# Kernel optimization log

Hardware: AMD Instinct MI355X
Metric: run time of the kernel (lower is better)

Reference implementation:

```python
import jax, jax.numpy as jnp
import numpy as np

N_NODES = 200000
N_EDGES = 3200000
N_GRAPHS = 64
IN_DIM, HIDDEN, OUT_DIM = 128, 16, 64


def setup_inputs() -> dict:
    key = jax.random.key(0)
    ks = jax.random.split(key, 5)
    x = jax.random.normal(ks[0], (N_NODES, IN_DIM), dtype=jnp.float32)
    edge_index = jax.random.randint(ks[1], (2, N_EDGES), 0, N_NODES, dtype=jnp.int64)
    batch = jnp.sort(jax.random.randint(ks[2], (N_NODES,), 0, N_GRAPHS, dtype=jnp.int64))
    W1 = jax.random.normal(ks[3], (IN_DIM, HIDDEN), dtype=jnp.float32) * (1.0 / np.sqrt(IN_DIM))
    W2 = jax.random.normal(ks[4], (HIDDEN, OUT_DIM), dtype=jnp.float32) * (1.0 / np.sqrt(HIDDEN))
    b1 = jnp.zeros((HIDDEN,), jnp.float32)
    b2 = jnp.zeros((OUT_DIM,), jnp.float32)
    return {"x": x, "edge_index": edge_index, "batch": batch,
            "W1": W1, "b1": b1, "W2": W2, "b2": b2, "training": 0}


def _gcn_conv(x, W, b, row, col, n_nodes):
    # PyG GCNConv: add-self-loop symmetric normalization, transform then
    # gather-from-row / scatter-add-to-col.  (row, col) already include self-loops.
    h = x @ W                                             # [N, out]
    deg = jnp.zeros((n_nodes,), h.dtype).at[col].add(1.0)  # degree incl. self-loop (>=1)
    dinv = deg ** -0.5
    norm = dinv[row] * dinv[col]                          # [E+N]
    out = jnp.zeros((n_nodes, W.shape[1]), h.dtype).at[col].add(h[row] * norm[:, None])
    return out + b


def reference(x, edge_index, batch, W1, b1, W2, b2, training):
    n = x.shape[0]
    loops = jnp.arange(n, dtype=edge_index.dtype)
    row = jnp.concatenate([edge_index[0], loops])
    col = jnp.concatenate([edge_index[1], loops])
    h = _gcn_conv(x, W1, b1, row, col, n)
    h = jax.nn.relu(h)
    # F.dropout with training=False is identity (reference is deterministic)
    h = _gcn_conv(h, W2, b2, row, col, n)
    # per-graph sum pooling: replaces the Python torch.where loop
    graph_embeds = jax.ops.segment_sum(h, batch, num_segments=N_GRAPHS)
    return graph_embeds
```

## Files before the change

kernel.cpp:

```cpp
#include <hip/hip_runtime.h>


#define TPB 256
#define CHUNK 4096
#define BK_SHIFT 9
#define NPB 512
#define W1S 20

__device__ __forceinline__ float bf2f(unsigned short u) {
    union { unsigned int i; float f; } v; v.i = ((unsigned int)u) << 16; return v.f;
}
__device__ __forceinline__ unsigned short f2bf(float f) {
    union { float f; unsigned int i; } v; v.f = f;
    unsigned int r = v.i + 0x7fff + ((v.i >> 16) & 1);
    return (unsigned short)(r >> 16);
}
__device__ __forceinline__ void bfacc8(uint4 v, unsigned int m, float* a) {
    union { unsigned int i; float f; } lo, hi;
    v.x &= m; v.y &= m; v.z &= m; v.w &= m;
    lo.i = v.x << 16; hi.i = v.x & 0xffff0000u; a[0] += lo.f; a[1] += hi.f;
    lo.i = v.y << 16; hi.i = v.y & 0xffff0000u; a[2] += lo.f; a[3] += hi.f;
    lo.i = v.z << 16; hi.i = v.z & 0xffff0000u; a[4] += lo.f; a[5] += hi.f;
    lo.i = v.w << 16; hi.i = v.w & 0xffff0000u; a[6] += lo.f; a[7] += hi.f;
}
__device__ __forceinline__ void bfunp8(uint4 v, float* a) {
    union { unsigned int i; float f; } lo, hi;
    lo.i = v.x << 16; hi.i = v.x & 0xffff0000u; a[0] = lo.f; a[1] = hi.f;
    lo.i = v.y << 16; hi.i = v.y & 0xffff0000u; a[2] = lo.f; a[3] = hi.f;
    lo.i = v.z << 16; hi.i = v.z & 0xffff0000u; a[4] = lo.f; a[5] = hi.f;
    lo.i = v.w << 16; hi.i = v.w & 0xffff0000u; a[6] = lo.f; a[7] = hi.f;
}

__global__ __launch_bounds__(TPB) void hist_kernel(const int* __restrict__ col,
                                                   int* __restrict__ counts,
                                                   int E, int nblk, int nbuck) {
    __shared__ int hist[512];
    int t = threadIdx.x;
    for (int i = t; i < nbuck; i += TPB) hist[i] = 0;
    __syncthreads();
    int e0 = blockIdx.x * CHUNK;
    for (int i = t; i < CHUNK; i += TPB) {
        int e = e0 + i;
        if (e < E) atomicAdd(&hist[col[e] >> BK_SHIFT], 1);
    }
    __syncthreads();
    for (int i = t; i < nbuck; i += TPB) counts[i * nblk + blockIdx.x] = hist[i];
}

__global__ __launch_bounds__(TPB) void scan1_kernel(const int* __restrict__ in,
                                                    int* __restrict__ out,
                                                    int* __restrict__ bsum, int L) {
    __shared__ int s[TPB];
    int t = threadIdx.x;
    int i = blockIdx.x * TPB + t;
    int d = (i < L) ? in[i] : 0;
    s[t] = d; __syncthreads();
    for (int off = 1; off < TPB; off <<= 1) {
        int v = (t >= off) ? s[t - off] : 0;
        __syncthreads();
        s[t] += v;
        __syncthreads();
    }
    if (i < L) out[i] = s[t] - d;
    if (t == TPB - 1) bsum[blockIdx.x] = s[t];
}

__global__ __launch_bounds__(1024) void scan2_kernel(int* __restrict__ bsum, int nb) {
    __shared__ int s[1024];
    int t = threadIdx.x;
    int i0 = t * 2, i1 = t * 2 + 1;
    int v0 = (i0 < nb) ? bsum[i0] : 0;
    int v1 = (i1 < nb) ? bsum[i1] : 0;
    int pv = v0 + v1;
    s[t] = pv; __syncthreads();
    for (int off = 1; off < 1024; off <<= 1) {
        int u = (t >= off) ? s[t - off] : 0;
        __syncthreads();
        s[t] += u;
        __syncthreads();
    }
    int exc = s[t] - pv;
    if (i0 < nb) bsum[i0] = exc;
    if (i1 < nb) bsum[i1] = exc + v0;
}

__device__ __forceinline__ int cbase_at(const int* counts, const int* bsum, int f) {
    return counts[f] + bsum[f >> 8];
}

__global__ __launch_bounds__(TPB) void s1c_gemm_kernel(
        const int* __restrict__ row, const int* __restrict__ col,
        const int* __restrict__ counts, const int* __restrict__ bsum,
        int E, int nblk, int nbuck,
        int* __restrict__ bucketed,
        const float* __restrict__ x, const float* __restrict__ W1,
        unsigned short* __restrict__ h1b, int N, int nbg) {
    __shared__ __align__(16) char sbuf[2048 + 2048 + 8192 + 64];
    int* slhist = (int*)sbuf;
    int* sgd    = (int*)(sbuf + 2048);
    unsigned short* ssidx = (unsigned short*)(sbuf + 4096);
    int* swtot  = (int*)(sbuf + 4096 + 8192);
    float* w1s  = (float*)sbuf;

    int b = (int)blockIdx.x, t = threadIdx.x;
    int M = min(nblk, nbg);
    int role, id;
    if (b < 2 * M) { role = b & 1; id = b >> 1; }
    else           { role = (nblk > nbg) ? 0 : 1; id = b - M; }

    if (role == 0) {
        int e0 = id * CHUNK;
        int nE = min(CHUNK, E - e0);
        int Ltot = nbuck * nblk;
        int lane = t & 63, w = t >> 6;
        int bk0 = 2 * t, bk1 = 2 * t + 1;
        int cb0 = 0, cb1 = 0, c0 = 0, c1 = 0;
        if (bk0 < nbuck) {
            int f = bk0 * nblk + id;
            cb0 = cbase_at(counts, bsum, f);
            int nx = (f + 1 < Ltot) ? cbase_at(counts, bsum, f + 1) : E;
            c0 = nx - cb0;
        }
        if (bk1 < nbuck) {
            int f = bk1 * nblk + id;
            cb1 = cbase_at(counts, bsum, f);
            int nx = (f + 1 < Ltot) ? cbase_at(counts, bsum, f + 1) : E;
            c1 = nx - cb1;
        }
        int s = c0 + c1;
        int v = s;
#pragma unroll
        for (int d = 1; d < 64; d <<= 1) {
            int u2 = __shfl_up(v, d, 64);
            if (lane >= d) v += u2;
        }
        if (lane == 63) swtot[w] = v;
        __syncthreads();
        int wbase = 0;
#pragma unroll
        for (int i = 0; i < 4; ++i) wbase += (i < w) ? swtot[i] : 0;
        int o0 = wbase + v - s;
        int o1 = o0 + c0;
        if (bk0 < nbuck) { slhist[bk0] = o0; sgd[bk0] = cb0 - o0; }
        if (bk1 < nbuck) { slhist[bk1] = o1; sgd[bk1] = cb1 - o1; }
        __syncthreads();
        for (int i = t; i < nE; i += TPB) {
            int c = col[e0 + i];
            int lp = atomicAdd(&slhist[c >> BK_SHIFT], 1);
            ssidx[lp] = (unsigned short)i;
        }
        __syncthreads();
        for (int j = t; j < nE; j += TPB) {
            int i = ssidx[j];
            int c = col[e0 + i];
            int r = row[e0 + i];
            bucketed[sgd[c >> BK_SHIFT] + j] = ((c & (NPB - 1)) << 18) | r;
        }
        return;
    }
    for (int i = t; i < 128 * 16; i += TPB)
        w1s[(i >> 4) * W1S + (i & 15)] = W1[i];
    __syncthreads();
    int g = t >> 2, q = t & 3;
    int n = id * 64 + g;
    int nc = min(n, N - 1);
    const float4* xr = (const float4*)(x + (size_t)nc * 128);
    float4 xv[8];
#pragma unroll
    for (int i = 0; i < 8; ++i) xv[i] = xr[i * 4 + q];
    float acc[16];
#pragma unroll
    for (int k = 0; k < 16; ++k) acc[k] = 0.f;
#pragma unroll
    for (int i = 0; i < 8; ++i) {
        float xj[4] = {xv[i].x, xv[i].y, xv[i].z, xv[i].w};
#pragma unroll
        for (int j = 0; j < 4; ++j) {
            int k = i * 16 + q * 4 + j;
            const float4* w4 = (const float4*)&w1s[k * W1S];
            float4 wa = w4[0], wb = w4[1], wc = w4[2], wd = w4[3];
            float xc = xj[j];
            acc[0]  = fmaf(xc, wa.x, acc[0]);  acc[1]  = fmaf(xc, wa.y, acc[1]);
            acc[2]  = fmaf(xc, wa.z, acc[2]);  acc[3]  = fmaf(xc, wa.w, acc[3]);
            acc[4]  = fmaf(xc, wb.x, acc[4]);  acc[5]  = fmaf(xc, wb.y, acc[5]);
            acc[6]  = fmaf(xc, wb.z, acc[6]);  acc[7]  = fmaf(xc, wb.w, acc[7]);
            acc[8]  = fmaf(xc, wc.x, acc[8]);  acc[9]  = fmaf(xc, wc.y, acc[9]);
            acc[10] = fmaf(xc, wc.z, acc[10]); acc[11] = fmaf(xc, wc.w, acc[11]);
            acc[12] = fmaf(xc, wd.x, acc[12]); acc[13] = fmaf(xc, wd.y, acc[13]);
            acc[14] = fmaf(xc, wd.z, acc[14]); acc[15] = fmaf(xc, wd.w, acc[15]);
        }
    }
#pragma unroll
    for (int d = 1; d < 4; d <<= 1) {
#pragma unroll
        for (int k = 0; k < 16; ++k) acc[k] += __shfl_xor(acc[k], d, 4);
    }
    if (n < N) {
        unsigned int u0 = (unsigned int)f2bf(acc[4 * q]) |
                          ((unsigned int)f2bf(acc[4 * q + 1]) << 16);
        unsigned int u1 = (unsigned int)f2bf(acc[4 * q + 2]) |
                          ((unsigned int)f2bf(acc[4 * q + 3]) << 16);
        *(uint2*)&h1b[(size_t)n * 16 + 4 * q] = make_uint2(u0, u1);
    }
}

__global__ __launch_bounds__(TPB) void sort_kernel(
        const int* __restrict__ bucketed,
        const int* __restrict__ counts, const int* __restrict__ bsum,
        int E, int nblk, int nbuck,
        int* __restrict__ csr, int* __restrict__ offs, float* __restrict__ dinv,
        const unsigned short* __restrict__ h1b, unsigned short* __restrict__ h1p, int N) {
    __shared__ int lhist[NPB];
    __shared__ int part[TPB];
    __shared__ float sdinv[NPB];
    int bk = blockIdx.x, t = threadIdx.x;
    int n0 = bk << BK_SHIFT;
    int n1 = min(n0 + NPB, N);
    int e0 = cbase_at(counts, bsum, bk * nblk);
    int e1 = (bk + 1 < nbuck) ? cbase_at(counts, bsum, (bk + 1) * nblk) : E;

    lhist[t] = 0; lhist[t + TPB] = 0;
    __syncthreads();
    for (int i = e0 + t; i < e1; i += TPB)
        atomicAdd(&lhist[bucketed[i] >> 18], 1);
    __syncthreads();

    int base = t * 2;
    int c0 = lhist[base], c1 = lhist[base + 1];
    int s = c0 + c1;
    part[t] = s;
    __syncthreads();
    for (int off = 1; off < TPB; off <<= 1) {
        int v = (t >= off) ? part[t - off] : 0;
        __syncthreads();
        part[t] += v;
        __syncthreads();
    }
    int o0 = e0 + part[t] - s;
    int o1 = o0 + c0;
    lhist[base] = o0; lhist[base + 1] = o1;
    sdinv[base]     = rsqrtf((float)c0 + 1.0f);
    sdinv[base + 1] = rsqrtf((float)c1 + 1.0f);
    int n = n0 + base;
    if (n + 0 < N) { offs[n + 0] = o0; dinv[n + 0] = sdinv[base]; }
    if (n + 1 < N) { offs[n + 1] = o1; dinv[n + 1] = sdinv[base + 1]; }
    __syncthreads();

    for (int i = e0 + t; i < e1; i += TPB) {
        int v = bucketed[i];
        int pos = atomicAdd(&lhist[v >> 18], 1);
        csr[pos] = v & 0x3FFFF;
    }
    int nq = (n1 - n0) * 4;
    for (int i = t; i < nq; i += TPB) {
        float dv = sdinv[i >> 2];
        uint2 u = ((const uint2*)h1b)[(size_t)n0 * 4 + i];
        float f0 = bf2f((unsigned short)(u.x & 0xffff));
        float f1 = bf2f((unsigned short)(u.x >> 16));
        float f2 = bf2f((unsigned short)(u.y & 0xffff));
        float f3 = bf2f((unsigned short)(u.y >> 16));
        ((ushort4*)h1p)[(size_t)n0 * 4 + i] =
            make_ushort4(f2bf(f0 * dv), f2bf(f1 * dv), f2bf(f2 * dv), f2bf(f3 * dv));
    }
    if (bk == 0 && t == 0) offs[N] = E;
}

__global__ __launch_bounds__(TPB) void gather1_kernel(const int* __restrict__ csr,
                                                      const int* __restrict__ offs,
                                                      const unsigned short* __restrict__ h1p,
                                                      const float* __restrict__ dinv,
                                                      const float* __restrict__ b1,
                                                      unsigned short* __restrict__ h2p, int N) {
    int t = threadIdx.x;
    int c = blockIdx.x * 16 + (t >> 4);
    int l = t & 15;
    int half = l & 1;
    int sub  = l >> 1;
    if (c >= N) return;
    int p0 = offs[c], p1 = offs[c + 1];
    float a[8];
#pragma unroll
    for (int k = 0; k < 8; ++k) a[k] = 0.f;
    for (int p = p0; p < p1; p += 16) {
        int s16 = csr[min(p + l, p1 - 1)];
#pragma unroll
        for (int h = 0; h < 2; ++h) {
            int e = 8 * h + sub;
            int src = __shfl(s16, e, 16);
            unsigned int m = ((p + e) < p1) ? 0xffffffffu : 0u;
            uint4 v = *(const uint4*)&h1p[(size_t)src * 16 + 8 * half];
            bfacc8(v, m, a);
        }
    }
#pragma unroll
    for (int d = 2; d < 16; d <<= 1) {
#pragma unroll
        for (int k = 0; k < 8; ++k) a[k] += __shfl_xor(a[k], d, 16);
    }
    if (l < 2) {
        float dc = dinv[c];
        uint4 sv = *(const uint4*)&h1p[(size_t)c * 16 + 8 * l];
        float sf[8];
        bfunp8(sv, sf);
        unsigned int uo[4];
#pragma unroll
        for (int q = 0; q < 4; ++q) {
            float r0 = fmaf(dc, a[2 * q] + sf[2 * q], b1[8 * l + 2 * q]);
            float r1 = fmaf(dc, a[2 * q + 1] + sf[2 * q + 1], b1[8 * l + 2 * q + 1]);
            r0 = dc * fmaxf(r0, 0.f);
            r1 = dc * fmaxf(r1, 0.f);
            uo[q] = (unsigned int)f2bf(r0) | ((unsigned int)f2bf(r1) << 16);
        }
        *(uint4*)&h2p[(size_t)c * 16 + 8 * l] = make_uint4(uo[0], uo[1], uo[2], uo[3]);
    }
}

__global__ __launch_bounds__(TPB) void gather2f_kernel(
        const int* __restrict__ csr, const int* __restrict__ offs,
        const unsigned short* __restrict__ h2p, const float* __restrict__ dinv,
        const float* __restrict__ W2, const float* __restrict__ b2,
        const int* __restrict__ batch, float* __restrict__ out, int N) {
    __shared__ float w2s[16 * 64];
    __shared__ float asT[64 * 17];
    __shared__ float pool[64];
    int t = threadIdx.x;
    for (int i = t; i < 16 * 64; i += TPB) w2s[i] = W2[i];
    if (t < 64) pool[t] = 0.f;

    int n0 = blockIdx.x * 64;
    int nLast = min(n0 + 63, N - 1);
    int g0 = batch[n0];
    bool uniform = (batch[nLast] == g0);

    int grp = t >> 4, l = t & 15;
    int half = l & 1, sub = l >> 1;
#pragma unroll 1
    for (int it = 0; it < 4; ++it) {
        int m = grp * 4 + it;
        int c = n0 + m;
        if (c < N) {
            int p0 = offs[c], p1 = offs[c + 1];
            float a[8];
#pragma unroll
            for (int k = 0; k < 8; ++k) a[k] = 0.f;
            for (int p = p0; p < p1; p += 16) {
                int s16 = csr[min(p + l, p1 - 1)];
#pragma unroll
                for (int h = 0; h < 2; ++h) {
                    int e = 8 * h + sub;
                    int src = __shfl(s16, e, 16);
                    unsigned int mm = ((p + e) < p1) ? 0xffffffffu : 0u;
                    uint4 v = *(const uint4*)&h2p[(size_t)src * 16 + 8 * half];
                    bfacc8(v, mm, a);
                }
            }
#pragma unroll
            for (int d = 2; d < 16; d <<= 1) {
#pragma unroll
                for (int k = 0; k < 8; ++k) a[k] += __shfl_xor(a[k], d, 16);
            }
            if (l < 2) {
                float dc = dinv[c];
                uint4 sv = *(const uint4*)&h2p[(size_t)c * 16 + 8 * l];
                float sf[8];
                bfunp8(sv, sf);
#pragma unroll
                for (int k = 0; k < 8; ++k)
                    asT[m * 17 + 8 * l + k] = dc * (a[k] + sf[k]);
            }
        }
    }
    __syncthreads();

    int wave = t >> 6, j = t & 63;
    float w2reg[16];
#pragma unroll
    for (int kx = 0; kx < 16; ++kx) w2reg[kx] = w2s[kx * 64 + j];
    float b2j = b2[j];
    float val = 0.f;
    int g_cur = -1;
#pragma unroll 1
    for (int mi = 0; mi < 16; ++mi) {
        int m = wave * 16 + mi;
        int c = n0 + m;
        if (c >= N) break;
        const float* ar = &asT[m * 17];
        float y = b2j;
#pragma unroll
        for (int kx = 0; kx < 16; ++kx) y = fmaf(ar[kx], w2reg[kx], y);
        if (uniform) {
            val += y;
        } else {
            int g = batch[c];
            if (g != g_cur) {
                if (g_cur >= 0) atomicAdd(&out[(size_t)g_cur * 64 + j], val);
                val = 0.f;
                g_cur = g;
            }
            val += y;
        }
    }
    if (uniform) {
        atomicAdd(&pool[j], val);
        __syncthreads();
        if (t < 64) atomicAdd(&out[(size_t)g0 * 64 + t], pool[t]);
    } else {
        if (g_cur >= 0) atomicAdd(&out[(size_t)g_cur * 64 + j], val);
    }
}

static inline size_t align64(size_t v) { return (v + 63) & ~(size_t)63; }

extern "C" void kernel_launch(void* const* d_in, const int* in_sizes, int n_in,
                              void* d_out, int out_size, void* d_ws, size_t ws_size,
                              hipStream_t stream) {
    const float* x     = (const float*)d_in[0];
    const int*   ei    = (const int*)d_in[1];
    const int*   batch = (const int*)d_in[2];
    const float* W1    = (const float*)d_in[3];
    const float* b1    = (const float*)d_in[4];
    const float* W2    = (const float*)d_in[5];
    const float* b2    = (const float*)d_in[6];

    const int N = in_sizes[0] / 128;
    const int E = in_sizes[1] / 2;
    const int* row = ei;
    const int* col = ei + E;

    const int NBLK  = (E + CHUNK - 1) / CHUNK;
    const int NBUCK = (N + NPB - 1) / NPB;
    const int L     = NBUCK * NBLK;
    const int NBS   = (L + TPB - 1) / TPB;
    const int NBG   = (N + 63) / 64;

    char* p = (char*)d_ws;
    int*            counts   = (int*)p;            p += align64((size_t)L * 4);
    int*            bsum     = (int*)p;            p += align64(2048 * 4);
    int*            bucketed = (int*)p;            p += align64((size_t)E * 4);
    int*            csr      = (int*)p;            p += align64((size_t)E * 4);
    int*            offs     = (int*)p;            p += align64((size_t)(N + 1) * 4);
    float*          dinv     = (float*)p;          p += align64((size_t)N * 4);
    unsigned short* h1b      = (unsigned short*)p; p += align64((size_t)N * 16 * 2);
    unsigned short* h1p      = (unsigned short*)p; p += align64((size_t)N * 16 * 2);
    unsigned short* h2p      = (unsigned short*)p; p += align64((size_t)N * 16 * 2);
    float*          out      = (float*)d_out;

    hipMemsetAsync(out, 0, (size_t)out_size * sizeof(float), stream);

    hist_kernel<<<NBLK, TPB, 0, stream>>>(col, counts, E, NBLK, NBUCK);
    scan1_kernel<<<NBS, TPB, 0, stream>>>(counts, counts, bsum, L);
    scan2_kernel<<<1, 1024, 0, stream>>>(bsum, NBS);
    s1c_gemm_kernel<<<NBLK + NBG, TPB, 0, stream>>>(row, col, counts, bsum,
                                                    E, NBLK, NBUCK,
                                                    bucketed, x, W1, h1b, N, NBG);
    sort_kernel<<<NBUCK, TPB, 0, stream>>>(bucketed, counts, bsum, E, NBLK, NBUCK,
                                           csr, offs, dinv, h1b, h1p, N);
    gather1_kernel<<<(N + 15) / 16, TPB, 0, stream>>>(csr, offs, h1p, dinv, b1, h2p, N);
    gather2f_kernel<<<(N + 63) / 64, TPB, 0, stream>>>(csr, offs, h2p, dinv,
                                                       W2, b2, batch, out, N);
}
```

Baseline: 342.6 us.

## Split fused scatter/GEMM kernel into separate launches and process two nodes per thread

The interleaved role-dispatch kernel, which ran the edge bucket scatter and the x@W1 GEMM in one launch, becomes two kernels launched back to back on the same stream. The GEMM kernel now computes two nodes per thread group (128 nodes per block), which halves the W1 shared-memory staging per node and doubles the loads in flight per thread. This gives up the concurrency of the fused launch, adds launch overhead, and raises register pressure in the GEMM.

```diff
diff --git a/kernel.cpp b/kernel.cpp
--- a/kernel.cpp
+++ b/kernel.cpp
@@ -88,119 +88,136 @@
     return counts[f] + bsum[f >> 8];
 }
 
-__global__ __launch_bounds__(TPB) void s1c_gemm_kernel(
+__global__ __launch_bounds__(TPB) void scatter_kernel(
         const int* __restrict__ row, const int* __restrict__ col,
         const int* __restrict__ counts, const int* __restrict__ bsum,
         int E, int nblk, int nbuck,
-        int* __restrict__ bucketed,
+        int* __restrict__ bucketed) {
+    __shared__ int slhist[512];
+    __shared__ int sgd[512];
+    __shared__ unsigned short ssidx[CHUNK];
+    __shared__ int swtot[4];
+    int id = (int)blockIdx.x, t = threadIdx.x;
+    int e0 = id * CHUNK;
+    int nE = min(CHUNK, E - e0);
+    int Ltot = nbuck * nblk;
+    int lane = t & 63, w = t >> 6;
+    int bk0 = 2 * t, bk1 = 2 * t + 1;
+    int cb0 = 0, cb1 = 0, c0 = 0, c1 = 0;
+    if (bk0 < nbuck) {
+        int f = bk0 * nblk + id;
+        cb0 = cbase_at(counts, bsum, f);
+        int nx = (f + 1 < Ltot) ? cbase_at(counts, bsum, f + 1) : E;
+        c0 = nx - cb0;
+    }
+    if (bk1 < nbuck) {
+        int f = bk1 * nblk + id;
+        cb1 = cbase_at(counts, bsum, f);
+        int nx = (f + 1 < Ltot) ? cbase_at(counts, bsum, f + 1) : E;
+        c1 = nx - cb1;
+    }
+    int s = c0 + c1;
+    int v = s;
+#pragma unroll
+    for (int d = 1; d < 64; d <<= 1) {
+        int u2 = __shfl_up(v, d, 64);
+        if (lane >= d) v += u2;
+    }
+    if (lane == 63) swtot[w] = v;
+    __syncthreads();
+    int wbase = 0;
+#pragma unroll
+    for (int i = 0; i < 4; ++i) wbase += (i < w) ? swtot[i] : 0;
+    int o0 = wbase + v - s;
+    int o1 = o0 + c0;
+    if (bk0 < nbuck) { slhist[bk0] = o0; sgd[bk0] = cb0 - o0; }
+    if (bk1 < nbuck) { slhist[bk1] = o1; sgd[bk1] = cb1 - o1; }
+    __syncthreads();
+    for (int i = t; i < nE; i += TPB) {
+        int c = col[e0 + i];
+        int lp = atomicAdd(&slhist[c >> BK_SHIFT], 1);
+        ssidx[lp] = (unsigned short)i;
+    }
+    __syncthreads();
+    for (int j = t; j < nE; j += TPB) {
+        int i = ssidx[j];
+        int c = col[e0 + i];
+        int r = row[e0 + i];
+        bucketed[sgd[c >> BK_SHIFT] + j] = ((c & (NPB - 1)) << 18) | r;
+    }
+}
+
+__global__ __launch_bounds__(TPB) void gemm_kernel(
         const float* __restrict__ x, const float* __restrict__ W1,
-        unsigned short* __restrict__ h1b, int N, int nbg) {
-    __shared__ __align__(16) char sbuf[2048 + 2048 + 8192 + 64];
-    int* slhist = (int*)sbuf;
-    int* sgd    = (int*)(sbuf + 2048);
-    unsigned short* ssidx = (unsigned short*)(sbuf + 4096);
-    int* swtot  = (int*)(sbuf + 4096 + 8192);
-    float* w1s  = (float*)sbuf;
-
-    int b = (int)blockIdx.x, t = threadIdx.x;
-    int M = min(nblk, nbg);
-    int role, id;
-    if (b < 2 * M) { role = b & 1; id = b >> 1; }
-    else           { role = (nblk > nbg) ? 0 : 1; id = b - M; }
-
-    if (role == 0) {
-        int e0 = id * CHUNK;
-        int nE = min(CHUNK, E - e0);
-        int Ltot = nbuck * nblk;
-        int lane = t & 63, w = t >> 6;
-        int bk0 = 2 * t, bk1 = 2 * t + 1;
-        int cb0 = 0, cb1 = 0, c0 = 0, c1 = 0;
-        if (bk0 < nbuck) {
-            int f = bk0 * nblk + id;
-            cb0 = cbase_at(counts, bsum, f);
-            int nx = (f + 1 < Ltot) ? cbase_at(counts, bsum, f + 1) : E;
-            c0 = nx - cb0;
-        }
-        if (bk1 < nbuck) {
-            int f = bk1 * nblk + id;
-            cb1 = cbase_at(counts, bsum, f);
-            int nx = (f + 1 < Ltot) ? cbase_at(counts, bsum, f + 1) : E;
-            c1 = nx - cb1;
-        }
-        int s = c0 + c1;
-        int v = s;
-#pragma unroll
-        for (int d = 1; d < 64; d <<= 1) {
-            int u2 = __shfl_up(v, d, 64);
-            if (lane >= d) v += u2;
-        }
-        if (lane == 63) swtot[w] = v;
-        __syncthreads();
-        int wbase = 0;
-#pragma unroll
-        for (int i = 0; i < 4; ++i) wbase += (i < w) ? swtot[i] : 0;
-        int o0 = wbase + v - s;
-        int o1 = o0 + c0;
-        if (bk0 < nbuck) { slhist[bk0] = o0; sgd[bk0] = cb0 - o0; }
-        if (bk1 < nbuck) { slhist[bk1] = o1; sgd[bk1] = cb1 - o1; }
-        __syncthreads();
-        for (int i = t; i < nE; i += TPB) {
-            int c = col[e0 + i];
-            int lp = atomicAdd(&slhist[c >> BK_SHIFT], 1);
-            ssidx[lp] = (unsigned short)i;
-        }
-        __syncthreads();
-        for (int j = t; j < nE; j += TPB) {
-            int i = ssidx[j];
-            int c = col[e0 + i];
-            int r = row[e0 + i];
-            bucketed[sgd[c >> BK_SHIFT] + j] = ((c & (NPB - 1)) << 18) | r;
-        }
-        return;
-    }
+        unsigned short* __restrict__ h1b, int N) {
+    __shared__ float w1s[128 * W1S];
+    int t = threadIdx.x;
     for (int i = t; i < 128 * 16; i += TPB)
         w1s[(i >> 4) * W1S + (i & 15)] = W1[i];
     __syncthreads();
     int g = t >> 2, q = t & 3;
-    int n = id * 64 + g;
-    int nc = min(n, N - 1);
-    const float4* xr = (const float4*)(x + (size_t)nc * 128);
-    float4 xv[8];
-#pragma unroll
-    for (int i = 0; i < 8; ++i) xv[i] = xr[i * 4 + q];
-    float acc[16];
-#pragma unroll
-    for (int k = 0; k < 16; ++k) acc[k] = 0.f;
+    int nA = (int)blockIdx.x * 128 + g;
+    int nB = nA + 64;
+    int nAc = min(nA, N - 1), nBc = min(nB, N - 1);
+    const float4* xA = (const float4*)(x + (size_t)nAc * 128);
+    const float4* xB = (const float4*)(x + (size_t)nBc * 128);
+    float4 xvA[8], xvB[8];
+#pragma unroll
+    for (int i = 0; i < 8; ++i) xvA[i] = xA[i * 4 + q];
+#pragma unroll
+    for (int i = 0; i < 8; ++i) xvB[i] = xB[i * 4 + q];
+    float accA[16], accB[16];
+#pragma unroll
+    for (int k = 0; k < 16; ++k) { accA[k] = 0.f; accB[k] = 0.f; }
 #pragma unroll
     for (int i = 0; i < 8; ++i) {
-        float xj[4] = {xv[i].x, xv[i].y, xv[i].z, xv[i].w};
+        float xjA[4] = {xvA[i].x, xvA[i].y, xvA[i].z, xvA[i].w};
+        float xjB[4] = {xvB[i].x, xvB[i].y, xvB[i].z, xvB[i].w};
 #pragma unroll
         for (int j = 0; j < 4; ++j) {
             int k = i * 16 + q * 4 + j;
             const float4* w4 = (const float4*)&w1s[k * W1S];
             float4 wa = w4[0], wb = w4[1], wc = w4[2], wd = w4[3];
-            float xc = xj[j];
-            acc[0]  = fmaf(xc, wa.x, acc[0]);  acc[1]  = fmaf(xc, wa.y, acc[1]);
-            acc[2]  = fmaf(xc, wa.z, acc[2]);  acc[3]  = fmaf(xc, wa.w, acc[3]);
-            acc[4]  = fmaf(xc, wb.x, acc[4]);  acc[5]  = fmaf(xc, wb.y, acc[5]);
-            acc[6]  = fmaf(xc, wb.z, acc[6]);  acc[7]  = fmaf(xc, wb.w, acc[7]);
-            acc[8]  = fmaf(xc, wc.x, acc[8]);  acc[9]  = fmaf(xc, wc.y, acc[9]);
-            acc[10] = fmaf(xc, wc.z, acc[10]); acc[11] = fmaf(xc, wc.w, acc[11]);
-            acc[12] = fmaf(xc, wd.x, acc[12]); acc[13] = fmaf(xc, wd.y, acc[13]);
-            acc[14] = fmaf(xc, wd.z, acc[14]); acc[15] = fmaf(xc, wd.w, acc[15]);
+            float xa = xjA[j], xb = xjB[j];
+            accA[0]  = fmaf(xa, wa.x, accA[0]);  accA[1]  = fmaf(xa, wa.y, accA[1]);
+            accA[2]  = fmaf(xa, wa.z, accA[2]);  accA[3]  = fmaf(xa, wa.w, accA[3]);
+            accA[4]  = fmaf(xa, wb.x, accA[4]);  accA[5]  = fmaf(xa, wb.y, accA[5]);
+            accA[6]  = fmaf(xa, wb.z, accA[6]);  accA[7]  = fmaf(xa, wb.w, accA[7]);
+            accA[8]  = fmaf(xa, wc.x, accA[8]);  accA[9]  = fmaf(xa, wc.y, accA[9]);
+            accA[10] = fmaf(xa, wc.z, accA[10]); accA[11] = fmaf(xa, wc.w, accA[11]);
+            accA[12] = fmaf(xa, wd.x, accA[12]); accA[13] = fmaf(xa, wd.y, accA[13]);
+            accA[14] = fmaf(xa, wd.z, accA[14]); accA[15] = fmaf(xa, wd.w, accA[15]);
+            accB[0]  = fmaf(xb, wa.x, accB[0]);  accB[1]  = fmaf(xb, wa.y, accB[1]);
+            accB[2]  = fmaf(xb, wa.z, accB[2]);  accB[3]  = fmaf(xb, wa.w, accB[3]);
+            accB[4]  = fmaf(xb, wb.x, accB[4]);  accB[5]  = fmaf(xb, wb.y, accB[5]);
+            accB[6]  = fmaf(xb, wb.z, accB[6]);  accB[7]  = fmaf(xb, wb.w, accB[7]);
+            accB[8]  = fmaf(xb, wc.x, accB[8]);  accB[9]  = fmaf(xb, wc.y, accB[9]);
+            accB[10] = fmaf(xb, wc.z, accB[10]); accB[11] = fmaf(xb, wc.w, accB[11]);
+            accB[12] = fmaf(xb, wd.x, accB[12]); accB[13] = fmaf(xb, wd.y, accB[13]);
+            accB[14] = fmaf(xb, wd.z, accB[14]); accB[15] = fmaf(xb, wd.w, accB[15]);
         }
     }
 #pragma unroll
     for (int d = 1; d < 4; d <<= 1) {
 #pragma unroll
-        for (int k = 0; k < 16; ++k) acc[k] += __shfl_xor(acc[k], d, 4);
-    }
-    if (n < N) {
-        unsigned int u0 = (unsigned int)f2bf(acc[4 * q]) |
-                          ((unsigned int)f2bf(acc[4 * q + 1]) << 16);
-        unsigned int u1 = (unsigned int)f2bf(acc[4 * q + 2]) |
-                          ((unsigned int)f2bf(acc[4 * q + 3]) << 16);
-        *(uint2*)&h1b[(size_t)n * 16 + 4 * q] = make_uint2(u0, u1);
+        for (int k = 0; k < 16; ++k) {
+            accA[k] += __shfl_xor(accA[k], d, 4);
+            accB[k] += __shfl_xor(accB[k], d, 4);
+        }
+    }
+    if (nA < N) {
+        unsigned int u0 = (unsigned int)f2bf(accA[4 * q]) |
+                          ((unsigned int)f2bf(accA[4 * q + 1]) << 16);
+        unsigned int u1 = (unsigned int)f2bf(accA[4 * q + 2]) |
+                          ((unsigned int)f2bf(accA[4 * q + 3]) << 16);
+        *(uint2*)&h1b[(size_t)nA * 16 + 4 * q] = make_uint2(u0, u1);
+    }
+    if (nB < N) {
+        unsigned int u0 = (unsigned int)f2bf(accB[4 * q]) |
+                          ((unsigned int)f2bf(accB[4 * q + 1]) << 16);
+        unsigned int u1 = (unsigned int)f2bf(accB[4 * q + 2]) |
+                          ((unsigned int)f2bf(accB[4 * q + 3]) << 16);
+        *(uint2*)&h1b[(size_t)nB * 16 + 4 * q] = make_uint2(u0, u1);
     }
 }
 
@@ -431,7 +448,7 @@
     const int NBUCK = (N + NPB - 1) / NPB;
     const int L     = NBUCK * NBLK;
     const int NBS   = (L + TPB - 1) / TPB;
-    const int NBG   = (N + 63) / 64;
+    const int NG2   = (N + 127) / 128;
 
     char* p = (char*)d_ws;
     int*            counts   = (int*)p;            p += align64((size_t)L * 4);
@@ -450,9 +467,9 @@
     hist_kernel<<<NBLK, TPB, 0, stream>>>(col, counts, E, NBLK, NBUCK);
     scan1_kernel<<<NBS, TPB, 0, stream>>>(counts, counts, bsum, L);
     scan2_kernel<<<1, 1024, 0, stream>>>(bsum, NBS);
-    s1c_gemm_kernel<<<NBLK + NBG, TPB, 0, stream>>>(row, col, counts, bsum,
-                                                    E, NBLK, NBUCK,
-                                                    bucketed, x, W1, h1b, N, NBG);
+    scatter_kernel<<<NBLK, TPB, 0, stream>>>(row, col, counts, bsum,
+                                             E, NBLK, NBUCK, bucketed);
+    gemm_kernel<<<NG2, TPB, 0, stream>>>(x, W1, h1b, N);
     sort_kernel<<<NBUCK, TPB, 0, stream>>>(bucketed, counts, bsum, E, NBLK, NBUCK,
                                            csr, offs, dinv, h1b, h1p, N);
     gather1_kernel<<<(N + 15) / 16, TPB, 0, stream>>>(csr, offs, h1p, dinv, b1, h2p, N);
```

Result: no change. 344.0 us (+0.4%).
